# Optimization experiments

Measured on AMD Instinct MI355X. Metric: run time of the kernel, lower is better.

## Reference

```python
import jax, jax.numpy as jnp
import numpy as np

B, T, N, D = 4, 8, 512, 512
K, dh = 8, 64  # D == K * dh
EMB = 64
EPS = 1e-5


def _layernorm(x, g, b):
    mu = jnp.mean(x, axis=-1, keepdims=True)
    var = jnp.mean(jnp.square(x - mu), axis=-1, keepdims=True)
    return (x - mu) * jax.lax.rsqrt(var + EPS) * g + b


def setup_inputs() -> dict:
    key = jax.random.key(0)
    ks = jax.random.split(key, 16)
    s = 1.0 / np.sqrt(D)
    x = jax.random.normal(ks[0], (B, T, N, D), jnp.float32)
    # sparse-ish Laplacian so the adjacency mask (-1e9 where lap==0) is exercised
    lap_dense = jax.random.normal(ks[1], (N, N), jnp.float32)
    keep = jax.random.uniform(ks[2], (N, N)) < 0.1
    lapmatrix = jnp.where(keep, lap_dense, 0.0)
    node_embeddings = jax.random.normal(ks[3], (N, EMB), jnp.float32)
    inp = {
        "x": x,
        "lapmatrix": lapmatrix,
        "node_embeddings": node_embeddings,
        "Wq": jax.random.normal(ks[4], (D, D), jnp.float32) * s,
        "bq": jnp.zeros((D,), jnp.float32),
        "Wk": jax.random.normal(ks[5], (D, D), jnp.float32) * s,
        "bk": jnp.zeros((D,), jnp.float32),
        "Wv": jax.random.normal(ks[6], (D, D), jnp.float32) * s,
        "bv": jnp.zeros((D,), jnp.float32),
        "ln1_g": jnp.ones((D,), jnp.float32),
        "ln1_b": jnp.zeros((D,), jnp.float32),
        "ln2_g": jnp.ones((D,), jnp.float32),
        "ln2_b": jnp.zeros((D,), jnp.float32),
        "alpha": jnp.float32(1.0),
        "beta": jnp.float32(1.0),
        "Wo": jax.random.normal(ks[7], (D, D), jnp.float32) * s,
        "bo": jnp.zeros((D,), jnp.float32),
        "W1": jax.random.normal(ks[8], (4 * D, D), jnp.float32) * s,
        "b1": jnp.zeros((4 * D,), jnp.float32),
        "W2": jax.random.normal(ks[9], (D, 4 * D), jnp.float32) * (1.0 / np.sqrt(4 * D)),
        "b2": jnp.zeros((D,), jnp.float32),
        "k": 3,
    }
    return inp


def reference(x, lapmatrix, node_embeddings, Wq, bq, Wk, bk, Wv, bv,
              ln1_g, ln1_b, ln2_g, ln2_b, alpha, beta, Wo, bo,
              W1, b1, W2, b2, k):
    # k is an unused forward arg in the original module; dropout is eval-mode identity.
    b_, t_, n_, d_ = x.shape
    xn = _layernorm(x, ln1_g, ln1_b)
    q = xn @ Wq.T + bq  # [B,T,N,D]
    ky = xn @ Wk.T + bk
    v = xn @ Wv.T + bv
    # [B,T,N,K,dh] -> [B,T,K,N,dh]
    q = q.reshape(b_, t_, n_, K, dh).transpose(0, 1, 3, 2, 4)
    ky = ky.reshape(b_, t_, n_, K, dh).transpose(0, 1, 3, 2, 4)
    v = v.reshape(b_, t_, n_, K, dh).transpose(0, 1, 3, 2, 4)
    raw = jnp.einsum('btkne,btkme->btknm', q, ky) / jnp.sqrt(jnp.float32(dh))
    # graph biases (broadcast [N,N] over B,T,K instead of materializing expands)
    supports = jax.nn.softmax(jax.nn.relu(node_embeddings @ node_embeddings.T), axis=1)
    mask = jnp.where(lapmatrix != 0, 0.0, -1e9).astype(x.dtype)
    logits = raw + alpha * supports + beta * lapmatrix + mask
    attn = jax.nn.softmax(logits, axis=-1)
    out = jnp.einsum('btknm,btkme->btkne', attn, v)
    out = out.transpose(0, 1, 3, 2, 4).reshape(b_, t_, n_, d_)
    x1 = x + (out @ Wo.T + bo)
    h = jax.nn.relu(_layernorm(x1, ln2_g, ln2_b) @ W1.T + b1)
    return x1 + (h @ W2.T + b2)
```

## Files before the change

### kernel.cpp

```cpp
#include <hip/hip_runtime.h>

typedef __bf16 bf16x8 __attribute__((ext_vector_type(8)));
typedef unsigned short u16x8 __attribute__((ext_vector_type(8)));
typedef float f32x4 __attribute__((ext_vector_type(4)));
typedef unsigned short u16;

__device__ __forceinline__ float bf2f(u16 u) {
    union { unsigned int i; float f; } x; x.i = ((unsigned int)u) << 16; return x.f;
}
__device__ __forceinline__ u16 f2bf(float f) {
    union { float f; unsigned int i; } x; x.f = f;
    unsigned int u = x.i;
    unsigned int r = (u + 0x7FFFu + ((u >> 16) & 1u)) >> 16;
    return (u16)r;
}

#define GL16(g, l) __builtin_amdgcn_global_load_lds( \
    (__attribute__((address_space(1))) void*)(void*)(g), \
    (__attribute__((address_space(3))) void*)(void*)(l), 16, 0, 0)

__global__ __launch_bounds__(256)
void cvt6_kernel(const float* __restrict__ s0, const float* __restrict__ s1,
                 const float* __restrict__ s2, const float* __restrict__ s3,
                 const float* __restrict__ s4, const float* __restrict__ s5,
                 u16* __restrict__ d0, u16* __restrict__ d1, u16* __restrict__ d2,
                 u16* __restrict__ d3, u16* __restrict__ d4, u16* __restrict__ d5)
{
    int b = blockIdx.x;
    const float* s; u16* d; int base;
    if (b < 512) {
        int t = b >> 7, lb = b & 127;
        s = (t == 0) ? s0 : (t == 1) ? s1 : (t == 2) ? s2 : s3;
        d = (t == 0) ? d0 : (t == 1) ? d1 : (t == 2) ? d2 : d3;
        base = lb * 2048;
    } else if (b < 1024) { s = s4; d = d4; base = (b - 512) * 2048; }
    else                 { s = s5; d = d5; base = (b - 1024) * 2048; }
    int i = base + threadIdx.x * 8;
    float4 a = *(const float4*)&s[i];
    float4 c = *(const float4*)&s[i + 4];
    u16x8 o;
    o[0] = f2bf(a.x); o[1] = f2bf(a.y); o[2] = f2bf(a.z); o[3] = f2bf(a.w);
    o[4] = f2bf(c.x); o[5] = f2bf(c.y); o[6] = f2bf(c.z); o[7] = f2bf(c.w);
    *(u16x8*)&d[i] = o;
}

__global__ __launch_bounds__(256)
void bias_kernel(const float* __restrict__ E, const float* __restrict__ lap,
                 const float* __restrict__ alpha_p, const float* __restrict__ beta_p,
                 float* __restrict__ biasout)
{
    __shared__ float wred[8];
    int tid = threadIdx.x;
    int i = blockIdx.x;
    int lane = tid & 63, wave = tid >> 6;
    int j0 = tid, j1 = tid + 256;
    float s0 = 0.f, s1 = 0.f;
#pragma unroll
    for (int t4 = 0; t4 < 16; ++t4) {
        float4 a  = *(const float4*)&E[i * 64 + t4 * 4];
        float4 e0 = *(const float4*)&E[j0 * 64 + t4 * 4];
        float4 e1 = *(const float4*)&E[j1 * 64 + t4 * 4];
        s0 += a.x * e0.x + a.y * e0.y + a.z * e0.z + a.w * e0.w;
        s1 += a.x * e1.x + a.y * e1.y + a.z * e1.z + a.w * e1.w;
    }
    s0 = fmaxf(s0, 0.f); s1 = fmaxf(s1, 0.f);
    float m = fmaxf(s0, s1);
#pragma unroll
    for (int o = 32; o > 0; o >>= 1) m = fmaxf(m, __shfl_xor(m, o));
    if (lane == 0) wred[wave] = m;
    __syncthreads();
    m = fmaxf(fmaxf(wred[0], wred[1]), fmaxf(wred[2], wred[3]));
    float e0v = __expf(s0 - m), e1v = __expf(s1 - m);
    float sum = e0v + e1v;
#pragma unroll
    for (int o = 32; o > 0; o >>= 1) sum += __shfl_xor(sum, o);
    if (lane == 0) wred[4 + wave] = sum;
    __syncthreads();
    float inv = 1.f / (wred[4] + wred[5] + wred[6] + wred[7]);
    float alpha = alpha_p[0], beta = beta_p[0];
    float lv0 = lap[i * 512 + j0];
    float lv1 = lap[i * 512 + j1];
    biasout[i * 512 + j0] = alpha * (e0v * inv) + beta * lv0 + (lv0 != 0.f ? 0.f : -1e9f);
    biasout[i * 512 + j1] = alpha * (e1v * inv) + beta * lv1 + (lv1 != 0.f ? 0.f : -1e9f);
}

__global__ __launch_bounds__(256)
void ln_kernel(const float* __restrict__ X, const float* __restrict__ G,
               const float* __restrict__ Bb, u16* __restrict__ Y)
{
    int row = blockIdx.x * 4 + (threadIdx.x >> 6);
    int lane = threadIdx.x & 63;
    const float* xr = X + (size_t)row * 512 + lane * 8;
    float4 a = *(const float4*)xr;
    float4 b = *(const float4*)(xr + 4);
    float v[8] = {a.x, a.y, a.z, a.w, b.x, b.y, b.z, b.w};
    float s = 0.f, ss = 0.f;
#pragma unroll
    for (int i = 0; i < 8; i++) { s += v[i]; ss += v[i] * v[i]; }
#pragma unroll
    for (int o = 32; o > 0; o >>= 1) { s += __shfl_xor(s, o); ss += __shfl_xor(ss, o); }
    float mu = s * (1.f / 512.f);
    float var = ss * (1.f / 512.f) - mu * mu;
    float rstd = rsqrtf(var + 1e-5f);
    float4 g0 = *(const float4*)&G[lane * 8];
    float4 g1 = *(const float4*)&G[lane * 8 + 4];
    float4 b0 = *(const float4*)&Bb[lane * 8];
    float4 b1 = *(const float4*)&Bb[lane * 8 + 4];
    float gv[8] = {g0.x, g0.y, g0.z, g0.w, g1.x, g1.y, g1.z, g1.w};
    float bv[8] = {b0.x, b0.y, b0.z, b0.w, b1.x, b1.y, b1.z, b1.w};
    u16x8 out;
#pragma unroll
    for (int i = 0; i < 8; i++) out[i] = f2bf((v[i] - mu) * rstd * gv[i] + bv[i]);
    *(u16x8*)&Y[(size_t)row * 512 + lane * 8] = out;
}

__global__ __launch_bounds__(256)
void gemm_bt(const u16* __restrict__ A, const u16* __restrict__ W,
             const float* __restrict__ bias,
             u16* __restrict__ Cb, int M, int Kd, int Nout, int mode)
{
    __shared__ __align__(16) char smem[128 * 136 * 2];
    u16* lA = (u16*)smem;
    u16* lB = lA + 128 * 32;
    int tid = threadIdx.x;
    int lane = tid & 63, wave = tid >> 6;
    int wm = wave >> 1, wn = wave & 1;
    int bid = blockIdx.y * gridDim.x + blockIdx.x;
    int per = (gridDim.x * gridDim.y) >> 3;
    int lb  = (bid & 7) * per + (bid >> 3);
    int bx = lb % gridDim.x, by = lb / gridDim.x;
    int row0 = by * 128, col0 = bx * 128;
    int rl = lane & 15, kq = lane >> 4;
    f32x4 acc[4][4];
#pragma unroll
    for (int i = 0; i < 4; i++)
#pragma unroll
        for (int j = 0; j < 4; j++) acc[i][j] = (f32x4){0.f, 0.f, 0.f, 0.f};

    int c0 = tid,       sr0 = c0 >> 2, sc0 = (c0 & 3) * 8;
    int c1 = 256 + tid, sr1 = c1 >> 2, sc1 = (c1 & 3) * 8;
    const u16* Abase = A + (size_t)row0 * Kd;
    const u16* Wbase = W + (size_t)col0 * Kd;

    for (int k0 = 0; k0 < Kd; k0 += 32) {
        GL16(Abase + (size_t)sr0 * Kd + k0 + sc0, &lA[c0 * 8]);
        GL16(Abase + (size_t)sr1 * Kd + k0 + sc1, &lA[c1 * 8]);
        GL16(Wbase + (size_t)sr0 * Kd + k0 + sc0, &lB[c0 * 8]);
        GL16(Wbase + (size_t)sr1 * Kd + k0 + sc1, &lB[c1 * 8]);
        __syncthreads();
        bf16x8 af[4], bf[4];
#pragma unroll
        for (int i = 0; i < 4; i++) af[i] = *(const bf16x8*)&lA[(wm * 64 + i * 16 + rl) * 32 + kq * 8];
#pragma unroll
        for (int j = 0; j < 4; j++) bf[j] = *(const bf16x8*)&lB[(wn * 64 + j * 16 + rl) * 32 + kq * 8];
#pragma unroll
        for (int i = 0; i < 4; i++)
#pragma unroll
            for (int j = 0; j < 4; j++)
                acc[i][j] = __builtin_amdgcn_mfma_f32_16x16x32_bf16(af[i], bf[j], acc[i][j], 0, 0, 0);
        __syncthreads();
    }
    u16* lC = (u16*)smem;
#pragma unroll
    for (int j = 0; j < 4; j++) {
        int col = wn * 64 + j * 16 + rl;
        float bsv = bias[col0 + col];
#pragma unroll
        for (int i = 0; i < 4; i++) {
            int rb = wm * 64 + i * 16 + kq * 4;
#pragma unroll
            for (int r = 0; r < 4; r++) {
                float vo = acc[i][j][r] + bsv;
                if (mode == 1) vo = fmaxf(vo, 0.f);
                lC[(rb + r) * 136 + col] = f2bf(vo);
            }
        }
    }
    __syncthreads();
#pragma unroll
    for (int rep = 0; rep < 8; rep++) {
        int row = rep * 16 + (tid >> 4);
        int col8 = (tid & 15) * 8;
        *(u16x8*)&Cb[(size_t)(row0 + row) * Nout + col0 + col8] = *(const u16x8*)&lC[row * 136 + col8];
    }
}

__global__ __launch_bounds__(256)
void gemm_bt64(const u16* __restrict__ A, const u16* __restrict__ W,
               const float* __restrict__ bias, const float* __restrict__ resid,
               float* __restrict__ Cf, int M, int Kd, int Nout)
{
    __shared__ __align__(16) char smem[64 * 132 * 4];
    u16* lA = (u16*)smem;
    u16* lB = lA + 64 * 32;
    int tid = threadIdx.x;
    int lane = tid & 63, wave = tid >> 6;
    int wm = wave >> 1, wn = wave & 1;
    int bid = blockIdx.y * gridDim.x + blockIdx.x;
    int per = (gridDim.x * gridDim.y) >> 3;
    int lb  = (bid & 7) * per + (bid >> 3);
    int bx = lb % gridDim.x, by = lb / gridDim.x;
    int row0 = by * 64, col0 = bx * 128;
    int rl = lane & 15, kq = lane >> 4;
    f32x4 acc[2][4];
#pragma unroll
    for (int i = 0; i < 2; i++)
#pragma unroll
        for (int j = 0; j < 4; j++) acc[i][j] = (f32x4){0.f, 0.f, 0.f, 0.f};

    int cA = tid,       arow = cA >> 2, acol = (cA & 3) * 8;
    int c0 = tid,       sr0 = c0 >> 2, sc0 = (c0 & 3) * 8;
    int c1 = 256 + tid, sr1 = c1 >> 2, sc1 = (c1 & 3) * 8;
    const u16* Abase = A + (size_t)row0 * Kd;
    const u16* Wbase = W + (size_t)col0 * Kd;

    for (int k0 = 0; k0 < Kd; k0 += 32) {
        GL16(Abase + (size_t)arow * Kd + k0 + acol, &lA[cA * 8]);
        GL16(Wbase + (size_t)sr0 * Kd + k0 + sc0, &lB[c0 * 8]);
        GL16(Wbase + (size_t)sr1 * Kd + k0 + sc1, &lB[c1 * 8]);
        __syncthreads();
        bf16x8 af[2], bf[4];
#pragma unroll
        for (int i = 0; i < 2; i++) af[i] = *(const bf16x8*)&lA[(wm * 32 + i * 16 + rl) * 32 + kq * 8];
#pragma unroll
        for (int j = 0; j < 4; j++) bf[j] = *(const bf16x8*)&lB[(wn * 64 + j * 16 + rl) * 32 + kq * 8];
#pragma unroll
        for (int i = 0; i < 2; i++)
#pragma unroll
            for (int j = 0; j < 4; j++)
                acc[i][j] = __builtin_amdgcn_mfma_f32_16x16x32_bf16(af[i], bf[j], acc[i][j], 0, 0, 0);
        __syncthreads();
    }
    float* lC = (float*)smem;
#pragma unroll
    for (int j = 0; j < 4; j++) {
        int col = wn * 64 + j * 16 + rl;
        float bsv = bias[col0 + col];
#pragma unroll
        for (int i = 0; i < 2; i++) {
            int rb = wm * 32 + i * 16 + kq * 4;
#pragma unroll
            for (int r = 0; r < 4; r++)
                lC[(rb + r) * 132 + col] = acc[i][j][r] + bsv;
        }
    }
    __syncthreads();
#pragma unroll
    for (int rep = 0; rep < 8; rep++) {
        int row = rep * 8 + (tid >> 5);
        int col4 = (tid & 31) * 4;
        size_t idx = (size_t)(row0 + row) * Nout + col0 + col4;
        float4 rv = *(const float4*)&resid[idx];
        float4 cv = *(const float4*)&lC[row * 132 + col4];
        cv.x += rv.x; cv.y += rv.y; cv.z += rv.z; cv.w += rv.w;
        *(float4*)&Cf[idx] = cv;
    }
}

__global__ __launch_bounds__(256)
void gemm_qkv(const u16* __restrict__ A,
              const u16* __restrict__ W0, const u16* __restrict__ W1, const u16* __restrict__ W2,
              const float* __restrict__ b0, const float* __restrict__ b1, const float* __restrict__ b2,
              u16* __restrict__ C0, u16* __restrict__ C1, u16* __restrict__ C2)
{
    __shared__ __align__(16) char smem[128 * 136 * 2];
    u16* lA = (u16*)smem;
    u16* lB = lA + 128 * 32;
    const int Kd = 512, Nout = 512;
    int bid = blockIdx.y * gridDim.x + blockIdx.x;
    int per = (gridDim.x * gridDim.y) >> 3;
    int lb  = (bid & 7) * per + (bid >> 3);
    int rest = lb % 12, by = lb / 12;
    int sel = rest >> 2;
    const u16* W = (sel == 0) ? W0 : (sel == 1) ? W1 : W2;
    const float* bias = (sel == 0) ? b0 : (sel == 1) ? b1 : b2;
    u16* Cb = (sel == 0) ? C0 : (sel == 1) ? C1 : C2;
    int tid = threadIdx.x;
    int lane = tid & 63, wave = tid >> 6;
    int wm = wave >> 1, wn = wave & 1;
    int row0 = by * 128, col0 = (rest & 3) * 128;
    int rl = lane & 15, kq = lane >> 4;
    f32x4 acc[4][4];
#pragma unroll
    for (int i = 0; i < 4; i++)
#pragma unroll
        for (int j = 0; j < 4; j++) acc[i][j] = (f32x4){0.f, 0.f, 0.f, 0.f};
    int c0 = tid,       sr0 = c0 >> 2, sc0 = (c0 & 3) * 8;
    int c1 = 256 + tid, sr1 = c1 >> 2, sc1 = (c1 & 3) * 8;
    const u16* Abase = A + (size_t)row0 * Kd;
    const u16* Wbase = W + (size_t)col0 * Kd;
    for (int k0 = 0; k0 < Kd; k0 += 32) {
        GL16(Abase + (size_t)sr0 * Kd + k0 + sc0, &lA[c0 * 8]);
        GL16(Abase + (size_t)sr1 * Kd + k0 + sc1, &lA[c1 * 8]);
        GL16(Wbase + (size_t)sr0 * Kd + k0 + sc0, &lB[c0 * 8]);
        GL16(Wbase + (size_t)sr1 * Kd + k0 + sc1, &lB[c1 * 8]);
        __syncthreads();
        bf16x8 af[4], bf[4];
#pragma unroll
        for (int i = 0; i < 4; i++) af[i] = *(const bf16x8*)&lA[(wm * 64 + i * 16 + rl) * 32 + kq * 8];
#pragma unroll
        for (int j = 0; j < 4; j++) bf[j] = *(const bf16x8*)&lB[(wn * 64 + j * 16 + rl) * 32 + kq * 8];
#pragma unroll
        for (int i = 0; i < 4; i++)
#pragma unroll
            for (int j = 0; j < 4; j++)
                acc[i][j] = __builtin_amdgcn_mfma_f32_16x16x32_bf16(af[i], bf[j], acc[i][j], 0, 0, 0);
        __syncthreads();
    }
    u16* lC = (u16*)smem;
#pragma unroll
    for (int j = 0; j < 4; j++) {
        int col = wn * 64 + j * 16 + rl;
        float bsv = bias[col0 + col];
#pragma unroll
        for (int i = 0; i < 4; i++) {
            int rb = wm * 64 + i * 16 + kq * 4;
#pragma unroll
            for (int r = 0; r < 4; r++)
                lC[(rb + r) * 136 + col] = f2bf(acc[i][j][r] + bsv);
        }
    }
    __syncthreads();
#pragma unroll
    for (int rep = 0; rep < 8; rep++) {
        int row = rep * 16 + (tid >> 4);
        int col8 = (tid & 15) * 8;
        *(u16x8*)&Cb[(size_t)(row0 + row) * Nout + col0 + col8] = *(const u16x8*)&lC[row * 136 + col8];
    }
}

__global__ __launch_bounds__(256, 2)
void flash_attn(const u16* __restrict__ Q, const u16* __restrict__ Km,
                const u16* __restrict__ V, const float* __restrict__ biasP,
                u16* __restrict__ O)
{
    __shared__ __align__(16) u16 lQ[128 * 64];
    __shared__ __align__(16) u16 lPK[128 * 136];
    __shared__ __align__(16) unsigned int lVt[64 * 68];
    __shared__ float red[2 * 128];
    __shared__ float m_s[128], l_s[128], alpha_s[128], mnew_s[128];

    int tid = threadIdx.x, lane = tid & 63, wave = tid >> 6;
    int wm = wave >> 1, wn = wave & 1;
    int rl = lane & 15, kq = lane >> 4;
    int qt = blockIdx.x, h = blockIdx.y, bt = blockIdx.z;
    int qg0 = qt * 128;
    size_t hb = (size_t)bt * (512 * 512) + h * 64;
    const u16* Qbase = Q + hb + (size_t)qg0 * 512;
    const u16* Kb0   = Km + hb;
    const u16* Vb0   = V + hb;

#pragma unroll
    for (int rep = 0; rep < 4; ++rep) {
        int c = rep * 256 + tid;
        int qr = c >> 3, d0 = (c & 7) * 8;
        GL16(Qbase + (size_t)qr * 512 + d0, &lQ[c * 8]);
    }
    if (tid < 128) { m_s[tid] = -3.0e38f; l_s[tid] = 0.f; }
    __syncthreads();

    bf16x8 af[4][2];
#pragma unroll
    for (int i = 0; i < 4; i++)
#pragma unroll
        for (int s = 0; s < 2; s++)
            af[i][s] = *(const bf16x8*)&lQ[(wm * 64 + i * 16 + rl) * 64 + s * 32 + kq * 8];

    f32x4 o[4][2];
#pragma unroll
    for (int i = 0; i < 4; i++)
#pragma unroll
        for (int jj = 0; jj < 2; jj++) o[i][jj] = (f32x4){0.f, 0.f, 0.f, 0.f};

    for (int t = 0; t < 4; ++t) {
        int kv0 = t * 128;
        __syncthreads();
        const u16* Kbase = Kb0 + (size_t)kv0 * 512;
#pragma unroll
        for (int rep = 0; rep < 4; ++rep) {
            int c = rep * 256 + tid;
            int kv = c >> 3, d0 = (c & 7) * 8;
            GL16(Kbase + (size_t)kv * 512 + d0, &lPK[c * 8]);
        }
        const u16* Vbase = Vb0 + (size_t)kv0 * 512;
#pragma unroll
        for (int rep = 0; rep < 2; ++rep) {
            int idx = rep * 256 + tid;
            int p = idx & 63, e0 = (idx >> 6) * 8;
            const u16* vp0 = Vbase + (size_t)(2 * p) * 512 + e0;
            u16x8 v0 = *(const u16x8*)vp0;
            u16x8 v1 = *(const u16x8*)(vp0 + 512);
#pragma unroll
            for (int u = 0; u < 8; ++u)
                lVt[(e0 + u) * 68 + p] = (unsigned)v0[u] | ((unsigned)v1[u] << 16);
        }
        __syncthreads();

        f32x4 acc[4][4];
#pragma unroll
        for (int j = 0; j < 4; ++j) {
            bf16x8 bk0 = *(const bf16x8*)&lPK[(wn * 64 + j * 16 + rl) * 64 + kq * 8];
            bf16x8 bk1 = *(const bf16x8*)&lPK[(wn * 64 + j * 16 + rl) * 64 + 32 + kq * 8];
#pragma unroll
            for (int i = 0; i < 4; ++i) {
                acc[i][j] = __builtin_amdgcn_mfma_f32_16x16x32_bf16(af[i][0], bk0,
                            (f32x4){0.f, 0.f, 0.f, 0.f}, 0, 0, 0);
                acc[i][j] = __builtin_amdgcn_mfma_f32_16x16x32_bf16(af[i][1], bk1, acc[i][j], 0, 0, 0);
            }
        }
#pragma unroll
        for (int i = 0; i < 4; ++i)
#pragma unroll
            for (int j = 0; j < 4; ++j) {
                int colg = kv0 + wn * 64 + j * 16 + rl;
                const float* bp = biasP + (size_t)(qg0 + wm * 64 + i * 16 + kq * 4) * 512 + colg;
#pragma unroll
                for (int r = 0; r < 4; ++r)
                    acc[i][j][r] = acc[i][j][r] * 0.125f + bp[(size_t)r * 512];
            }

#pragma unroll
        for (int i = 0; i < 4; ++i) {
            float mx[4];
#pragma unroll
            for (int r = 0; r < 4; ++r) {
                mx[r] = fmaxf(fmaxf(acc[i][0][r], acc[i][1][r]), fmaxf(acc[i][2][r], acc[i][3][r]));
#pragma unroll
                for (int off = 8; off > 0; off >>= 1) mx[r] = fmaxf(mx[r], __shfl_xor(mx[r], off));
            }
            if (rl == 0) {
#pragma unroll
                for (int r = 0; r < 4; ++r)
                    red[wn * 128 + wm * 64 + i * 16 + kq * 4 + r] = mx[r];
            }
        }
        __syncthreads();
        if (tid < 128) {
            float pm = fmaxf(red[tid], red[128 + tid]);
            float mo = m_s[tid];
            float mn = fmaxf(mo, pm);
            m_s[tid] = mn; mnew_s[tid] = mn;
            alpha_s[tid] = __expf(mo - mn);
        }
        __syncthreads();

#pragma unroll
        for (int i = 0; i < 4; ++i) {
            int rb = wm * 64 + i * 16 + kq * 4;
            float mn[4], al[4], sm[4];
#pragma unroll
            for (int r = 0; r < 4; ++r) { mn[r] = mnew_s[rb + r]; al[r] = alpha_s[rb + r]; sm[r] = 0.f; }
#pragma unroll
            for (int j = 0; j < 4; ++j) {
                int col = wn * 64 + j * 16 + rl;
#pragma unroll
                for (int r = 0; r < 4; ++r) {
                    float p = __expf(acc[i][j][r] - mn[r]);
                    sm[r] += p;
                    lPK[(rb + r) * 136 + col] = f2bf(p);
                }
            }
#pragma unroll
            for (int jj = 0; jj < 2; ++jj)
#pragma unroll
                for (int r = 0; r < 4; ++r) o[i][jj][r] *= al[r];
#pragma unroll
            for (int r = 0; r < 4; ++r) {
#pragma unroll
                for (int off = 8; off > 0; off >>= 1) sm[r] += __shfl_xor(sm[r], off);
            }
            if (rl == 0) {
#pragma unroll
                for (int r = 0; r < 4; ++r) red[wn * 128 + rb + r] = sm[r];
            }
        }
        __syncthreads();
        if (tid < 128) l_s[tid] = l_s[tid] * alpha_s[tid] + red[tid] + red[128 + tid];

#pragma unroll
        for (int ks = 0; ks < 4; ++ks) {
            bf16x8 aP[4], bV[2];
#pragma unroll
            for (int i = 0; i < 4; ++i)
                aP[i] = *(const bf16x8*)&lPK[(wm * 64 + i * 16 + rl) * 136 + ks * 32 + kq * 8];
#pragma unroll
            for (int jj = 0; jj < 2; ++jj)
                bV[jj] = *(const bf16x8*)&lVt[(wn * 32 + jj * 16 + rl) * 68 + ks * 16 + kq * 4];
#pragma unroll
            for (int i = 0; i < 4; ++i)
#pragma unroll
                for (int jj = 0; jj < 2; ++jj)
                    o[i][jj] = __builtin_amdgcn_mfma_f32_16x16x32_bf16(aP[i], bV[jj], o[i][jj], 0, 0, 0);
        }
    }
    __syncthreads();

#pragma unroll
    for (int i = 0; i < 4; ++i) {
        int rb = wm * 64 + i * 16 + kq * 4;
        float il[4];
#pragma unroll
        for (int r = 0; r < 4; ++r) il[r] = 1.f / l_s[rb + r];
#pragma unroll
        for (int jj = 0; jj < 2; ++jj) {
            int e = wn * 32 + jj * 16 + rl;
#pragma unroll
            for (int r = 0; r < 4; ++r)
                lPK[(rb + r) * 136 + e] = f2bf(o[i][jj][r] * il[r]);
        }
    }
    __syncthreads();
    u16* Ob = O + hb + (size_t)qg0 * 512;
#pragma unroll
    for (int rep = 0; rep < 4; ++rep) {
        int row = rep * 32 + (tid >> 3);
        int col8 = (tid & 7) * 8;
        *(u16x8*)&Ob[(size_t)row * 512 + col8] = *(const u16x8*)&lPK[row * 136 + col8];
    }
}

extern "C" void kernel_launch(void* const* d_in, const int* in_sizes, int n_in,
                              void* d_out, int out_size, void* d_ws, size_t ws_size,
                              hipStream_t stream)
{
    const float* x     = (const float*)d_in[0];
    const float* lap   = (const float*)d_in[1];
    const float* emb   = (const float*)d_in[2];
    const float* Wq    = (const float*)d_in[3];
    const float* bq    = (const float*)d_in[4];
    const float* Wk    = (const float*)d_in[5];
    const float* bk    = (const float*)d_in[6];
    const float* Wv    = (const float*)d_in[7];
    const float* bvv   = (const float*)d_in[8];
    const float* g1    = (const float*)d_in[9];
    const float* bb1   = (const float*)d_in[10];
    const float* g2    = (const float*)d_in[11];
    const float* bb2   = (const float*)d_in[12];
    const float* alpha = (const float*)d_in[13];
    const float* beta  = (const float*)d_in[14];
    const float* Wo    = (const float*)d_in[15];
    const float* bo    = (const float*)d_in[16];
    const float* W1    = (const float*)d_in[17];
    const float* b1    = (const float*)d_in[18];
    const float* W2    = (const float*)d_in[19];
    const float* b2    = (const float*)d_in[20];
    float* out = (float*)d_out;

    const size_t SZ = (size_t)4 * 8 * 512 * 512;
    char* w = (char*)d_ws;
    float* bias = (float*)w;  w += (size_t)512 * 512 * 4;
    u16* wqb = (u16*)w; w += (size_t)512 * 512 * 2;
    u16* wkb = (u16*)w; w += (size_t)512 * 512 * 2;
    u16* wvb = (u16*)w; w += (size_t)512 * 512 * 2;
    u16* wob = (u16*)w; w += (size_t)512 * 512 * 2;
    u16* w1b = (u16*)w; w += (size_t)2048 * 512 * 2;
    u16* w2b = (u16*)w; w += (size_t)512 * 2048 * 2;
    u16* xnb = (u16*)w; w += SZ * 2;
    u16* qb  = (u16*)w; w += SZ * 2;
    u16* kb  = (u16*)w; w += SZ * 2;
    u16* vb  = (u16*)w; w += SZ * 2;
    u16* hb  = (u16*)w; w += (size_t)16384 * 2048 * 2;
    float* x1 = out;

    const int M = 16384;
    cvt6_kernel<<<1536, 256, 0, stream>>>(Wq, Wk, Wv, Wo, W1, W2,
                                          wqb, wkb, wvb, wob, w1b, w2b);
    bias_kernel<<<512, 256, 0, stream>>>(emb, lap, alpha, beta, bias);
    ln_kernel<<<M / 4, 256, 0, stream>>>(x, g1, bb1, xnb);
    gemm_qkv<<<dim3(12, 128), 256, 0, stream>>>(xnb, wqb, wkb, wvb, bq, bk, bvv, qb, kb, vb);
    flash_attn<<<dim3(4, 8, 32), 256, 0, stream>>>(qb, kb, vb, bias, xnb);
    gemm_bt64<<<dim3(4, 256), 256, 0, stream>>>(xnb, wob, bo, x, x1, M, 512, 512);
    ln_kernel<<<M / 4, 256, 0, stream>>>(x1, g2, bb2, qb);
    gemm_bt<<<dim3(16, 128), 256, 0, stream>>>(qb, w1b, b1, hb, M, 512, 2048, 1);
    gemm_bt64<<<dim3(4, 256), 256, 0, stream>>>(hb, w2b, b2, x1, out, M, 2048, 512);
}
```

Baseline: 389.4 us.

## Enlarge residual GEMM tiles, swizzle attention LDS, transpose bias, keep running max in registers

Several unrelated changes land together. The residual output GEMMs move from 64x128 to 128x128 tiles and write the epilogue directly from registers instead of staging through LDS. Flash attention gains XOR-swizzled LDS layouts for Q, K and transposed V to avoid bank conflicts, and shares memory between buffers so occupancy can rise to 3 blocks. It keeps the running row max in registers, which removes one barrier-plus-reduction step per KV tile. The bias matrix is stored transposed so each lane reads four consecutive rows as one float4 load. The cost is that the direct epilogue stores are strided and uncoalesced, and the larger GEMM tiles halve the number of blocks.

```diff
diff --git a/kernel.cpp b/kernel.cpp
--- a/kernel.cpp
+++ b/kernel.cpp
@@ -80,8 +80,8 @@
     float alpha = alpha_p[0], beta = beta_p[0];
     float lv0 = lap[i * 512 + j0];
     float lv1 = lap[i * 512 + j1];
-    biasout[i * 512 + j0] = alpha * (e0v * inv) + beta * lv0 + (lv0 != 0.f ? 0.f : -1e9f);
-    biasout[i * 512 + j1] = alpha * (e1v * inv) + beta * lv1 + (lv1 != 0.f ? 0.f : -1e9f);
+    biasout[j0 * 512 + i] = alpha * (e0v * inv) + beta * lv0 + (lv0 != 0.f ? 0.f : -1e9f);
+    biasout[j1 * 512 + i] = alpha * (e1v * inv) + beta * lv1 + (lv1 != 0.f ? 0.f : -1e9f);
 }
 
 __global__ __launch_bounds__(256)
@@ -186,13 +186,12 @@
 }
 
 __global__ __launch_bounds__(256)
-void gemm_bt64(const u16* __restrict__ A, const u16* __restrict__ W,
-               const float* __restrict__ bias, const float* __restrict__ resid,
-               float* __restrict__ Cf, int M, int Kd, int Nout)
-{
-    __shared__ __align__(16) char smem[64 * 132 * 4];
-    u16* lA = (u16*)smem;
-    u16* lB = lA + 64 * 32;
+void gemm128_res(const u16* __restrict__ A, const u16* __restrict__ W,
+                 const float* __restrict__ bias, const float* __restrict__ resid,
+                 float* __restrict__ Cf, int M, int Kd, int Nout)
+{
+    __shared__ __align__(16) u16 lA[128 * 32];
+    __shared__ __align__(16) u16 lB[128 * 32];
     int tid = threadIdx.x;
     int lane = tid & 63, wave = tid >> 6;
     int wm = wave >> 1, wn = wave & 1;
@@ -200,60 +199,50 @@
     int per = (gridDim.x * gridDim.y) >> 3;
     int lb  = (bid & 7) * per + (bid >> 3);
     int bx = lb % gridDim.x, by = lb / gridDim.x;
-    int row0 = by * 64, col0 = bx * 128;
+    int row0 = by * 128, col0 = bx * 128;
     int rl = lane & 15, kq = lane >> 4;
-    f32x4 acc[2][4];
-#pragma unroll
-    for (int i = 0; i < 2; i++)
+    f32x4 acc[4][4];
+#pragma unroll
+    for (int i = 0; i < 4; i++)
 #pragma unroll
         for (int j = 0; j < 4; j++) acc[i][j] = (f32x4){0.f, 0.f, 0.f, 0.f};
 
-    int cA = tid,       arow = cA >> 2, acol = (cA & 3) * 8;
     int c0 = tid,       sr0 = c0 >> 2, sc0 = (c0 & 3) * 8;
     int c1 = 256 + tid, sr1 = c1 >> 2, sc1 = (c1 & 3) * 8;
     const u16* Abase = A + (size_t)row0 * Kd;
     const u16* Wbase = W + (size_t)col0 * Kd;
 
     for (int k0 = 0; k0 < Kd; k0 += 32) {
-        GL16(Abase + (size_t)arow * Kd + k0 + acol, &lA[cA * 8]);
+        GL16(Abase + (size_t)sr0 * Kd + k0 + sc0, &lA[c0 * 8]);
+        GL16(Abase + (size_t)sr1 * Kd + k0 + sc1, &lA[c1 * 8]);
         GL16(Wbase + (size_t)sr0 * Kd + k0 + sc0, &lB[c0 * 8]);
         GL16(Wbase + (size_t)sr1 * Kd + k0 + sc1, &lB[c1 * 8]);
         __syncthreads();
-        bf16x8 af[2], bf[4];
-#pragma unroll
-        for (int i = 0; i < 2; i++) af[i] = *(const bf16x8*)&lA[(wm * 32 + i * 16 + rl) * 32 + kq * 8];
+        bf16x8 af[4], bf[4];
+#pragma unroll
+        for (int i = 0; i < 4; i++) af[i] = *(const bf16x8*)&lA[(wm * 64 + i * 16 + rl) * 32 + kq * 8];
 #pragma unroll
         for (int j = 0; j < 4; j++) bf[j] = *(const bf16x8*)&lB[(wn * 64 + j * 16 + rl) * 32 + kq * 8];
 #pragma unroll
-        for (int i = 0; i < 2; i++)
+        for (int i = 0; i < 4; i++)
 #pragma unroll
             for (int j = 0; j < 4; j++)
                 acc[i][j] = __builtin_amdgcn_mfma_f32_16x16x32_bf16(af[i], bf[j], acc[i][j], 0, 0, 0);
         __syncthreads();
     }
-    float* lC = (float*)smem;
 #pragma unroll
     for (int j = 0; j < 4; j++) {
-        int col = wn * 64 + j * 16 + rl;
-        float bsv = bias[col0 + col];
-#pragma unroll
-        for (int i = 0; i < 2; i++) {
-            int rb = wm * 32 + i * 16 + kq * 4;
-#pragma unroll
-            for (int r = 0; r < 4; r++)
-                lC[(rb + r) * 132 + col] = acc[i][j][r] + bsv;
-        }
-    }
-    __syncthreads();
-#pragma unroll
-    for (int rep = 0; rep < 8; rep++) {
-        int row = rep * 8 + (tid >> 5);
-        int col4 = (tid & 31) * 4;
-        size_t idx = (size_t)(row0 + row) * Nout + col0 + col4;
-        float4 rv = *(const float4*)&resid[idx];
-        float4 cv = *(const float4*)&lC[row * 132 + col4];
-        cv.x += rv.x; cv.y += rv.y; cv.z += rv.z; cv.w += rv.w;
-        *(float4*)&Cf[idx] = cv;
+        int col = col0 + wn * 64 + j * 16 + rl;
+        float bsv = bias[col];
+#pragma unroll
+        for (int i = 0; i < 4; i++) {
+            int rb = row0 + wm * 64 + i * 16 + kq * 4;
+#pragma unroll
+            for (int r = 0; r < 4; r++) {
+                size_t idx = (size_t)(rb + r) * Nout + col;
+                Cf[idx] = acc[i][j][r] + bsv + resid[idx];
+            }
+        }
     }
 }
 
@@ -329,16 +318,19 @@
     }
 }
 
-__global__ __launch_bounds__(256, 2)
+__global__ __launch_bounds__(256, 3)
 void flash_attn(const u16* __restrict__ Q, const u16* __restrict__ Km,
-                const u16* __restrict__ V, const float* __restrict__ biasP,
+                const u16* __restrict__ V, const float* __restrict__ biasT,
                 u16* __restrict__ O)
 {
-    __shared__ __align__(16) u16 lQ[128 * 64];
-    __shared__ __align__(16) u16 lPK[128 * 136];
-    __shared__ __align__(16) unsigned int lVt[64 * 68];
-    __shared__ float red[2 * 128];
-    __shared__ float m_s[128], l_s[128], alpha_s[128], mnew_s[128];
+    __shared__ __align__(16) char smem[54272];
+    u16* lPK      = (u16*)smem;
+    u16* lQ       = (u16*)(smem + 34816);
+    unsigned* lVt = (unsigned*)(smem + 34816);
+    float* red_m   = (float*)(smem + 51200);
+    float* red_s   = red_m + 256;
+    float* alpha_s = red_s + 256;
+    float* l_s     = alpha_s + 128;
 
     int tid = threadIdx.x, lane = tid & 63, wave = tid >> 6;
     int wm = wave >> 1, wn = wave & 1;
@@ -353,24 +345,32 @@
 #pragma unroll
     for (int rep = 0; rep < 4; ++rep) {
         int c = rep * 256 + tid;
-        int qr = c >> 3, d0 = (c & 7) * 8;
+        int qr = c >> 3, d0 = (((c & 7) ^ (qr & 7)) * 8);
         GL16(Qbase + (size_t)qr * 512 + d0, &lQ[c * 8]);
     }
-    if (tid < 128) { m_s[tid] = -3.0e38f; l_s[tid] = 0.f; }
+    if (tid < 128) l_s[tid] = 0.f;
     __syncthreads();
 
     bf16x8 af[4][2];
 #pragma unroll
-    for (int i = 0; i < 4; i++)
-#pragma unroll
-        for (int s = 0; s < 2; s++)
-            af[i][s] = *(const bf16x8*)&lQ[(wm * 64 + i * 16 + rl) * 64 + s * 32 + kq * 8];
-
+    for (int i = 0; i < 4; i++) {
+        int row = wm * 64 + i * 16 + rl;
+#pragma unroll
+        for (int s = 0; s < 2; s++) {
+            int sl = (s * 4 + kq) ^ (row & 7);
+            af[i][s] = *(const bf16x8*)&lQ[row * 64 + sl * 8];
+        }
+    }
+
+    float m_reg[4][4];
     f32x4 o[4][2];
 #pragma unroll
-    for (int i = 0; i < 4; i++)
+    for (int i = 0; i < 4; i++) {
+#pragma unroll
+        for (int r = 0; r < 4; r++) m_reg[i][r] = -3.0e38f;
 #pragma unroll
         for (int jj = 0; jj < 2; jj++) o[i][jj] = (f32x4){0.f, 0.f, 0.f, 0.f};
+    }
 
     for (int t = 0; t < 4; ++t) {
         int kv0 = t * 128;
@@ -379,7 +379,7 @@
 #pragma unroll
         for (int rep = 0; rep < 4; ++rep) {
             int c = rep * 256 + tid;
-            int kv = c >> 3, d0 = (c & 7) * 8;
+            int kv = c >> 3, d0 = (((c & 7) ^ (kv & 7)) * 8);
             GL16(Kbase + (size_t)kv * 512 + d0, &lPK[c * 8]);
         }
         const u16* Vbase = Vb0 + (size_t)kv0 * 512;
@@ -391,16 +391,21 @@
             u16x8 v0 = *(const u16x8*)vp0;
             u16x8 v1 = *(const u16x8*)(vp0 + 512);
 #pragma unroll
-            for (int u = 0; u < 8; ++u)
-                lVt[(e0 + u) * 68 + p] = (unsigned)v0[u] | ((unsigned)v1[u] << 16);
+            for (int u = 0; u < 8; ++u) {
+                int row = e0 + u;
+                int col = ((((p >> 2) ^ (row & 15)) << 2) | (p & 3));
+                lVt[row * 64 + col] = (unsigned)v0[u] | ((unsigned)v1[u] << 16);
+            }
         }
         __syncthreads();
 
         f32x4 acc[4][4];
 #pragma unroll
         for (int j = 0; j < 4; ++j) {
-            bf16x8 bk0 = *(const bf16x8*)&lPK[(wn * 64 + j * 16 + rl) * 64 + kq * 8];
-            bf16x8 bk1 = *(const bf16x8*)&lPK[(wn * 64 + j * 16 + rl) * 64 + 32 + kq * 8];
+            int row = wn * 64 + j * 16 + rl;
+            int sl0 = kq ^ (row & 7), sl1 = (4 + kq) ^ (row & 7);
+            bf16x8 bk0 = *(const bf16x8*)&lPK[row * 64 + sl0 * 8];
+            bf16x8 bk1 = *(const bf16x8*)&lPK[row * 64 + sl1 * 8];
 #pragma unroll
             for (int i = 0; i < 4; ++i) {
                 acc[i][j] = __builtin_amdgcn_mfma_f32_16x16x32_bf16(af[i][0], bk0,
@@ -409,16 +414,18 @@
             }
         }
 #pragma unroll
-        for (int i = 0; i < 4; ++i)
-#pragma unroll
-            for (int j = 0; j < 4; ++j) {
-                int colg = kv0 + wn * 64 + j * 16 + rl;
-                const float* bp = biasP + (size_t)(qg0 + wm * 64 + i * 16 + kq * 4) * 512 + colg;
+        for (int j = 0; j < 4; ++j) {
+            int colg = kv0 + wn * 64 + j * 16 + rl;
+            const float* bp = biasT + (size_t)colg * 512 + qg0;
+#pragma unroll
+            for (int i = 0; i < 4; ++i) {
+                float4 bv = *(const float4*)&bp[wm * 64 + i * 16 + kq * 4];
+                float bvr[4] = {bv.x, bv.y, bv.z, bv.w};
 #pragma unroll
                 for (int r = 0; r < 4; ++r)
-                    acc[i][j][r] = acc[i][j][r] * 0.125f + bp[(size_t)r * 512];
-            }
-
+                    acc[i][j][r] = acc[i][j][r] * 0.125f + bvr[r];
+            }
+        }
 #pragma unroll
         for (int i = 0; i < 4; ++i) {
             float mx[4];
@@ -429,18 +436,10 @@
                 for (int off = 8; off > 0; off >>= 1) mx[r] = fmaxf(mx[r], __shfl_xor(mx[r], off));
             }
             if (rl == 0) {
-#pragma unroll
-                for (int r = 0; r < 4; ++r)
-                    red[wn * 128 + wm * 64 + i * 16 + kq * 4 + r] = mx[r];
-            }
-        }
-        __syncthreads();
-        if (tid < 128) {
-            float pm = fmaxf(red[tid], red[128 + tid]);
-            float mo = m_s[tid];
-            float mn = fmaxf(mo, pm);
-            m_s[tid] = mn; mnew_s[tid] = mn;
-            alpha_s[tid] = __expf(mo - mn);
+                int rb = wm * 64 + i * 16 + kq * 4;
+#pragma unroll
+                for (int r = 0; r < 4; ++r) red_m[wn * 128 + rb + r] = mx[r];
+            }
         }
         __syncthreads();
 
@@ -449,7 +448,18 @@
             int rb = wm * 64 + i * 16 + kq * 4;
             float mn[4], al[4], sm[4];
 #pragma unroll
-            for (int r = 0; r < 4; ++r) { mn[r] = mnew_s[rb + r]; al[r] = alpha_s[rb + r]; sm[r] = 0.f; }
+            for (int r = 0; r < 4; ++r) {
+                float pm = fmaxf(red_m[rb + r], red_m[128 + rb + r]);
+                float mo = m_reg[i][r];
+                mn[r] = fmaxf(mo, pm);
+                al[r] = __expf(mo - mn[r]);
+                m_reg[i][r] = mn[r];
+                sm[r] = 0.f;
+            }
+            if (rl == 0 && wn == 0) {
+#pragma unroll
+                for (int r = 0; r < 4; ++r) alpha_s[rb + r] = al[r];
+            }
 #pragma unroll
             for (int j = 0; j < 4; ++j) {
                 int col = wn * 64 + j * 16 + rl;
@@ -471,11 +481,11 @@
             }
             if (rl == 0) {
 #pragma unroll
-                for (int r = 0; r < 4; ++r) red[wn * 128 + rb + r] = sm[r];
-            }
-        }
-        __syncthreads();
-        if (tid < 128) l_s[tid] = l_s[tid] * alpha_s[tid] + red[tid] + red[128 + tid];
+                for (int r = 0; r < 4; ++r) red_s[wn * 128 + rb + r] = sm[r];
+            }
+        }
+        __syncthreads();
+        if (tid < 128) l_s[tid] = l_s[tid] * alpha_s[tid] + red_s[tid] + red_s[128 + tid];
 
 #pragma unroll
         for (int ks = 0; ks < 4; ++ks) {
@@ -484,8 +494,11 @@
             for (int i = 0; i < 4; ++i)
                 aP[i] = *(const bf16x8*)&lPK[(wm * 64 + i * 16 + rl) * 136 + ks * 32 + kq * 8];
 #pragma unroll
-            for (int jj = 0; jj < 2; ++jj)
-                bV[jj] = *(const bf16x8*)&lVt[(wn * 32 + jj * 16 + rl) * 68 + ks * 16 + kq * 4];
+            for (int jj = 0; jj < 2; ++jj) {
+                int row = wn * 32 + jj * 16 + rl;
+                int sl = (ks * 4 + kq) ^ (row & 15);
+                bV[jj] = *(const bf16x8*)&lVt[row * 64 + sl * 4];
+            }
 #pragma unroll
             for (int i = 0; i < 4; ++i)
 #pragma unroll
@@ -569,8 +582,8 @@
     ln_kernel<<<M / 4, 256, 0, stream>>>(x, g1, bb1, xnb);
     gemm_qkv<<<dim3(12, 128), 256, 0, stream>>>(xnb, wqb, wkb, wvb, bq, bk, bvv, qb, kb, vb);
     flash_attn<<<dim3(4, 8, 32), 256, 0, stream>>>(qb, kb, vb, bias, xnb);
-    gemm_bt64<<<dim3(4, 256), 256, 0, stream>>>(xnb, wob, bo, x, x1, M, 512, 512);
+    gemm128_res<<<dim3(4, 128), 256, 0, stream>>>(xnb, wob, bo, x, x1, M, 512, 512);
     ln_kernel<<<M / 4, 256, 0, stream>>>(x1, g2, bb2, qb);
     gemm_bt<<<dim3(16, 128), 256, 0, stream>>>(qb, w1b, b1, hb, M, 512, 2048, 1);
-    gemm_bt64<<<dim3(4, 256), 256, 0, stream>>>(hb, w2b, b2, x1, out, M, 2048, 512);
-}
+    gemm128_res<<<dim3(4, 128), 256, 0, stream>>>(hb, w2b, b2, x1, out, M, 2048, 512);
+}
```

Result: slower. 554.8 us (+42.5%).
